# Optimization experiments

Measured on AMD Instinct MI355X. Metric: run time of the kernel, lower is better.

The kernel has to match this reference:

```python
import jax, jax.numpy as jnp
import numpy as np

NUM_JOINTS = 33
EPS = 1e-5
# MediaPipe 33-landmark pose skeleton connections
SKELETON_EDGES = np.array([
    [0,1],[1,2],[2,3],[3,7],[0,4],[4,5],[5,6],[6,8],[9,10],
    [11,12],[11,13],[13,15],[15,17],[15,19],[15,21],[17,19],
    [12,14],[14,16],[16,18],[16,20],[16,22],[18,20],
    [11,23],[12,24],[23,24],[23,25],[24,26],[25,27],[26,28],
    [27,29],[28,30],[29,31],[30,32],[27,31],[28,32]], dtype=np.int64)


def _batched_edges(B):
    und = np.concatenate([SKELETON_EDGES, SKELETON_EDGES[:, ::-1]], axis=0)
    loops = np.stack([np.arange(NUM_JOINTS)] * 2, axis=1)
    e = np.concatenate([und, loops], axis=0)  # [103, 2] per graph (incl. self loops)
    eb = (e[None, :, :] + (np.arange(B) * NUM_JOINTS)[:, None, None]).reshape(-1, 2)
    return jnp.asarray(eb[:, 0], dtype=jnp.int32), jnp.asarray(eb[:, 1], dtype=jnp.int32)


def setup_inputs() -> dict:
    key = jax.random.key(0)
    B, N, F, H, L = 4096, NUM_JOINTS, 256, 256, 4
    ks = jax.random.split(key, 20)
    d = {"x": jax.random.normal(ks[0], (B, N, F), dtype=jnp.float32)}
    dims = [(F, H), (H, H), (H, H)]
    i = 1
    for li, (di, do) in enumerate(dims):
        d[f"w{li}"] = jax.random.normal(ks[i], (di, do), dtype=jnp.float32) * 0.05; i += 1
        d[f"b{li}"] = jnp.zeros((do,), dtype=jnp.float32)
        d[f"g{li}"] = jnp.ones((do,), dtype=jnp.float32)
        d[f"be{li}"] = jnp.zeros((do,), dtype=jnp.float32)
    d["wh"] = jax.random.normal(ks[i], (H, H), dtype=jnp.float32) * 0.05; i += 1
    d["bh"] = jnp.zeros((H,), dtype=jnp.float32)
    d["wc"] = jax.random.normal(ks[i], (H, L), dtype=jnp.float32) * 0.05; i += 1
    d["bc"] = jnp.zeros((L,), dtype=jnp.float32)
    src, dst = _batched_edges(B)
    d["src"], d["dst"] = src, dst
    return d


def _gcn_conv(x, W, b, src, dst, norm, num_nodes):
    h = x @ W                          # [NN, out]
    msg = h[src] * norm[:, None]       # gather + scale
    agg = jax.ops.segment_sum(msg, dst, num_segments=num_nodes)
    return agg + b


def _bn_relu(x, g, be):
    mu = jnp.mean(x, axis=0)
    var = jnp.mean((x - mu) ** 2, axis=0)  # biased, torch training BN
    return jax.nn.relu((x - mu) * jax.lax.rsqrt(var + EPS) * g + be)


def reference(x, w0, b0, g0, be0, w1, b1, g1, be1, w2, b2, g2, be2, wh, bh, wc, bc, src, dst):
    B, N, F = x.shape
    NN = B * N
    h = jnp.nan_to_num(x.reshape(NN, F))
    # symmetric GCN normalization D^{-1/2}(A+I)D^{-1/2}; self loops already in edge list
    deg = jax.ops.segment_sum(jnp.ones_like(src, dtype=h.dtype), dst, num_segments=NN)
    dinv = jax.lax.rsqrt(deg)
    norm = dinv[src] * dinv[dst]
    for W, b, g, be in ((w0, b0, g0, be0), (w1, b1, g1, be1), (w2, b2, g2, be2)):
        h = _gcn_conv(h, W, b, src, dst, norm, NN)
        h = _bn_relu(h, g, be)  # dropout: eval mode -> identity
    h = _gcn_conv(h, wh, bh, src, dst, norm, NN)
    pooled = h.reshape(B, N, -1).mean(axis=1)  # global mean pool per graph
    return pooled @ wc + bc
```

## Files before the change

kernel.cpp:

```cpp
#include <hip/hip_runtime.h>

typedef unsigned short u16;
typedef __attribute__((ext_vector_type(8))) short short8;
typedef __attribute__((ext_vector_type(4))) float floatx4;

#define NN_TOT 135168

#define WAITVM(N) asm volatile("s_waitcnt vmcnt(" #N ")" ::: "memory")
#define WAITLGKM0 asm volatile("s_waitcnt lgkmcnt(0)" ::: "memory")

static constexpr int NBCNT[33] = {2,2,2,2,2,2,2,1,1,1,1,3,3,2,2,4,4,2,2,2,2,1,1,3,3,2,2,3,3,2,2,2,2};
static constexpr int NBR[33][4] = {
 {1,4,0,0},{0,2,0,0},{1,3,0,0},{2,7,0,0},{0,5,0,0},{4,6,0,0},{5,8,0,0},
 {3,0,0,0},{6,0,0,0},{10,0,0,0},{9,0,0,0},
 {12,13,23,0},{11,14,24,0},{11,15,0,0},{12,16,0,0},
 {13,17,19,21},{14,18,20,22},
 {15,19,0,0},{16,20,0,0},{15,17,0,0},{16,18,0,0},{15,0,0,0},{16,0,0,0},
 {11,24,25,0},{12,23,26,0},{23,27,0,0},{24,28,0,0},
 {25,29,31,0},{26,30,32,0},{27,31,0,0},{28,32,0,0},{29,27,0,0},{30,28,0,0}};
static constexpr float R2 = 0.70710678f, R3 = 0.57735027f, R4 = 0.5f, R5 = 0.44721360f;
static constexpr float DINV[33] = {R3,R3,R3,R3,R3,R3,R3, R2,R2,R2,R2, R4,R4, R3,R3, R5,R5,
                                   R3,R3,R3,R3, R2,R2, R4,R4, R3,R3, R4,R4, R3,R3,R3,R3};

__device__ __forceinline__ float bf2f(u16 u) {
  unsigned int v = ((unsigned int)u) << 16; float f; __builtin_memcpy(&f, &v, 4); return f;
}
__device__ __forceinline__ u16 f2bf(float f) {
  unsigned int u; __builtin_memcpy(&u, &f, 4);
  return (u16)((u + 0x7fffu + ((u >> 16) & 1u)) >> 16);
}
__device__ __forceinline__ float ldin(const void* p, int i, int isbf) {
  return isbf ? bf2f(((const u16*)p)[i]) : ((const float*)p)[i];
}
__device__ __forceinline__ void gload_lds16(const u16* g, u16* l) {
  __builtin_amdgcn_global_load_lds((const __attribute__((address_space(1))) unsigned int*)g,
                                   (__attribute__((address_space(3))) unsigned int*)l, 16, 0, 0);
}
__device__ __forceinline__ int lof(int row, int qq) {
  return row*32 + ((qq ^ ((row >> 1) & 3)) * 8);
}

__global__ __launch_bounds__(256) void detect_kernel(const u16* __restrict__ x,
                                                     int* __restrict__ flag)
{
  __shared__ int cnt[256];
  const int t = threadIdx.x;
  int c = 0;
  for (int j = 0; j < 16; ++j) {
    u16 u = x[(t*16 + j)*2];
    int e = (u >> 7) & 0xFF;
    c += (e >= 118 && e <= 130) ? 1 : 0;
  }
  cnt[t] = c;
  __syncthreads();
  if (t == 0) {
    int s = 0;
    for (int i = 0; i < 256; ++i) s += cnt[i];
    *flag = (s > 2048) ? 1 : 0;
  }
}

__global__ __launch_bounds__(256) void transpose_kernel(const void* __restrict__ w0,
    const void* __restrict__ w1, const void* __restrict__ w2, u16* __restrict__ Wt,
    const int* __restrict__ flag)
{
  const int m = blockIdx.x >> 4;
  const int nb = (blockIdx.x & 15) * 16;
  const void* W = m == 0 ? w0 : (m == 1 ? w1 : w2);
  u16* O = Wt + (size_t)m * 65536;
  const int t = threadIdx.x;
  const int lane = t & 63, wv = t >> 6;
  const int isbf = *flag;
  if (isbf) {
    const u16* Wb = (const u16*)W;
#pragma unroll
    for (int nn = 0; nn < 4; ++nn) {
      const int n = nb + nn*4 + wv;
#pragma unroll
      for (int j = 0; j < 4; ++j) {
        const int k = lane + 64*j;
        O[n*256 + k] = Wb[k*256 + n];
      }
    }
  } else {
    const float* Wf = (const float*)W;
#pragma unroll
    for (int nn = 0; nn < 4; ++nn) {
      const int n = nb + nn*4 + wv;
#pragma unroll
      for (int j = 0; j < 4; ++j) {
        const int k = lane + 64*j;
        O[n*256 + k] = f2bf(Wf[k*256 + n]);
      }
    }
  }
}

__global__ __launch_bounds__(256) void init_kernel(const void* __restrict__ wh,
    const void* __restrict__ bh, const void* __restrict__ wc, const void* __restrict__ bc,
    float* __restrict__ wq, float* __restrict__ bq, float* __restrict__ repl,
    const int* __restrict__ flag)
{
  const int idx = blockIdx.x*256 + threadIdx.x;
  for (int i = idx; i < 3*64*512; i += 65*256) repl[i] = 0.f;
  const int isbf = *flag;
  const int t = threadIdx.x;
  const int lane = t & 63;
  if (blockIdx.x < 64) {
    const int r = blockIdx.x*4 + (t >> 6);
    float a0=0.f, a1=0.f, a2=0.f, a3=0.f;
#pragma unroll
    for (int j = 0; j < 4; ++j) {
      const int k = lane + 64*j;
      const float w = ldin(wh, r*256 + k, isbf);
      a0 += w*ldin(wc, k*4+0, isbf); a1 += w*ldin(wc, k*4+1, isbf);
      a2 += w*ldin(wc, k*4+2, isbf); a3 += w*ldin(wc, k*4+3, isbf);
    }
#pragma unroll
    for (int off = 32; off; off >>= 1) {
      a0 += __shfl_xor(a0, off); a1 += __shfl_xor(a1, off);
      a2 += __shfl_xor(a2, off); a3 += __shfl_xor(a3, off);
    }
    if (lane == 0) { wq[r*4+0]=a0; wq[r*4+1]=a1; wq[r*4+2]=a2; wq[r*4+3]=a3; }
  } else if (t < 64) {
    float s0=0.f, s1=0.f, s2=0.f, s3=0.f;
#pragma unroll
    for (int j = 0; j < 4; ++j) {
      const int k = lane + 64*j;
      const float b = ldin(bh, k, isbf);
      s0 += b*ldin(wc, k*4+0, isbf); s1 += b*ldin(wc, k*4+1, isbf);
      s2 += b*ldin(wc, k*4+2, isbf); s3 += b*ldin(wc, k*4+3, isbf);
    }
#pragma unroll
    for (int off = 32; off; off >>= 1) {
      s0 += __shfl_xor(s0, off); s1 += __shfl_xor(s1, off);
      s2 += __shfl_xor(s2, off); s3 += __shfl_xor(s3, off);
    }
    if (lane == 0) {
      bq[0] = s0 + ldin(bc, 0, isbf); bq[1] = s1 + ldin(bc, 1, isbf);
      bq[2] = s2 + ldin(bc, 2, isbf); bq[3] = s3 + ldin(bc, 3, isbf);
    }
  }
}

template<int ACT>
__global__ __launch_bounds__(256, 2) void fused_kernel(
    const void* __restrict__ Ag, const u16* __restrict__ Bt,
    const float* __restrict__ fscale, const float* __restrict__ fshift,
    const void* __restrict__ bias, u16* __restrict__ H,
    float* __restrict__ repl, const int* __restrict__ flag)
{
  __shared__ __align__(16) u16 smem[22528];
  u16* const sA0 = smem;
  u16* const sA1 = smem + 3072;
  u16* const sB0 = smem + 6144;
  u16* const sB1 = smem + 14336;
  const int tid = threadIdx.x;
  const int lane = tid & 63, w = tid >> 6;
  const int gi = w >> 1, h = w & 1;
  const int fr = lane & 15, q = lane >> 4;
  const int lr = lane >> 2, cq = lane & 3;
  const int swz = (lr >> 1) & 3;
  const int r0 = tid >> 2;
  const int c8 = (tid & 3) * 8;
  const size_t R0 = (size_t)blockIdx.x * 66;
  const int dtf = *flag;
  const int isbf = (ACT == 0) ? dtf : 1;

  const u16* Ab = (const u16*)Ag;
  const float* Af = (const float*)Ag;

  floatx4 acc[3][8];
#pragma unroll
  for (int t = 0; t < 3; ++t)
#pragma unroll
    for (int j = 0; j < 8; ++j) acc[t][j] = (floatx4){0.f, 0.f, 0.f, 0.f};

  auto issueB = [&](u16* dst, int k0) {
#pragma unroll
    for (int i = 0; i < 4; ++i)
      gload_lds16(Bt + (w*64 + i*16 + lr)*256 + k0 + (cq ^ swz)*8,
                  dst + (w*64 + i*16)*32);
  };
  auto issueA_dma = [&](u16* dst, int k0) {
    gload_lds16(Ab + (R0 + w*16 + lr)*256 + k0 + (cq ^ swz)*8, dst + (w*16)*32);
    if (w == 0) {
      size_t rg = R0 + 64 + lr;
      if (rg >= NN_TOT) rg = NN_TOT - 1;
      gload_lds16(Ab + rg*256 + k0 + (cq ^ swz)*8, dst + 64*32);
    }
  };

  uint4 regA, regA2;
  float sc8[8], sh8[8];
  auto issueA_reg = [&](int k0) {
    float4 t0 = *(const float4*)(fscale + k0 + c8);
    float4 t1 = *(const float4*)(fscale + k0 + c8 + 4);
    float4 t2 = *(const float4*)(fshift + k0 + c8);
    float4 t3 = *(const float4*)(fshift + k0 + c8 + 4);
    sc8[0]=t0.x; sc8[1]=t0.y; sc8[2]=t0.z; sc8[3]=t0.w;
    sc8[4]=t1.x; sc8[5]=t1.y; sc8[6]=t1.z; sc8[7]=t1.w;
    sh8[0]=t2.x; sh8[1]=t2.y; sh8[2]=t2.z; sh8[3]=t2.w;
    sh8[4]=t3.x; sh8[5]=t3.y; sh8[6]=t3.z; sh8[7]=t3.w;
    regA = *(const uint4*)(Ab + (R0 + r0)*256 + k0 + c8);
    if (tid >= 248)
      regA2 = *(const uint4*)(Ab + (R0 + 64 + ((tid - 248) >> 2))*256 + k0 + c8);
  };
  auto writeA = [&](u16* dst) {
    {
      const u16* us = (const u16*)&regA;
      u16 ov[8];
#pragma unroll
      for (int j = 0; j < 8; ++j) {
        float f = bf2f(us[j]);
        f = fmaxf(0.f, fmaf(f, sc8[j], sh8[j]));
        ov[j] = f2bf(f);
      }
      *(uint4*)(dst + r0*32 + ((cq ^ ((r0 >> 1) & 3))*8)) = *(const uint4*)ov;
    }
    if (tid >= 248) {
      const int rr = 64 + ((tid - 248) >> 2);
      const u16* us = (const u16*)&regA2;
      u16 ov[8];
#pragma unroll
      for (int j = 0; j < 8; ++j) {
        float f = bf2f(us[j]);
        f = fmaxf(0.f, fmaf(f, sc8[j], sh8[j]));
        ov[j] = f2bf(f);
      }
      *(uint4*)(dst + rr*32 + ((cq ^ ((rr >> 1) & 3))*8)) = *(const uint4*)ov;
    }
  };

  auto compute = [&](const u16* cA, const u16* cB) {
    short8 a[3], b[8];
#pragma unroll
    for (int t = 0; t < 3; ++t)
      a[t] = *(const short8*)(cA + lof(gi*33 + t*16 + fr, q));
#pragma unroll
    for (int nf = 0; nf < 8; ++nf)
      b[nf] = *(const short8*)(cB + lof(h*128 + nf*16 + fr, q));
#pragma unroll
    for (int t = 0; t < 3; ++t)
#pragma unroll
      for (int nf = 0; nf < 8; ++nf)
        acc[t][nf] = __builtin_amdgcn_mfma_f32_16x16x32_bf16(a[t], b[nf], acc[t][nf], 0, 0, 0);
  };

  if (ACT == 0 && !isbf) {
    for (int kc = 0; kc < 8; ++kc) {
      const int k0 = kc * 32;
      __syncthreads();
      {
        const float* ap = Af + (R0 + r0)*256 + k0 + c8;
        float4 p0 = *(const float4*)(ap);
        float4 p1 = *(const float4*)(ap + 4);
        u16 ov[8];
        ov[0]=f2bf(p0.x); ov[1]=f2bf(p0.y); ov[2]=f2bf(p0.z); ov[3]=f2bf(p0.w);
        ov[4]=f2bf(p1.x); ov[5]=f2bf(p1.y); ov[6]=f2bf(p1.z); ov[7]=f2bf(p1.w);
        *(uint4*)(sA0 + r0*32 + ((cq ^ ((r0 >> 1) & 3))*8)) = *(const uint4*)ov;
      }
      if (tid < 8) {
        const int rr = 64 + (tid >> 2);
        const float* ap = Af + (R0 + rr)*256 + k0 + c8;
        float4 p0 = *(const float4*)(ap);
        float4 p1 = *(const float4*)(ap + 4);
        u16 ov[8];
        ov[0]=f2bf(p0.x); ov[1]=f2bf(p0.y); ov[2]=f2bf(p0.z); ov[3]=f2bf(p0.w);
        ov[4]=f2bf(p1.x); ov[5]=f2bf(p1.y); ov[6]=f2bf(p1.z); ov[7]=f2bf(p1.w);
        *(uint4*)(sA0 + rr*32 + ((cq ^ ((rr >> 1) & 3))*8)) = *(const uint4*)ov;
      }
      issueB(sB0, k0);
      __syncthreads();
      compute(sA0, sB0);
    }
  } else {
    if (ACT == 0) issueA_dma(sA0, 0); else issueA_reg(0);
    issueB(sB0, 0);
    if (ACT == 1) { WAITVM(4); writeA(sA0); WAITLGKM0; }

    for (int kc = 0; kc < 8; ++kc) {
      u16* curA = (kc & 1) ? sA1 : sA0;
      u16* nxtA = (kc & 1) ? sA0 : sA1;
      u16* curB = (kc & 1) ? sB1 : sB0;
      u16* nxtB = (kc & 1) ? sB0 : sB1;
      if (kc < 7) {
        if (ACT == 0) issueA_dma(nxtA, (kc + 1) * 32);
        else          issueA_reg((kc + 1) * 32);
        issueB(nxtB, (kc + 1) * 32);
      }
      if (kc < 7) {
        if (ACT == 0) { if (w == 0) { WAITVM(6); } else { WAITVM(5); } }
        else          { if (w == 3) { WAITVM(10); } else { WAITVM(9); } }
      } else { WAITVM(0); }
      __builtin_amdgcn_sched_barrier(0);
      __builtin_amdgcn_s_barrier();

      compute(curA, curB);

      if (ACT == 1 && kc < 7) { WAITVM(4); writeA(nxtA); }
      WAITLGKM0;
    }
  }

  __syncthreads();
  u16* const Tl = smem;
#pragma unroll
  for (int t = 0; t < 3; ++t)
#pragma unroll
    for (int nf = 0; nf < 8; ++nf)
#pragma unroll
      for (int r = 0; r < 4; ++r) {
        const int row = t*16 + q*4 + r;
        if (row < 33)
          Tl[(gi*33 + row)*264 + h*128 + nf*16 + fr] = f2bf(acc[t][nf][r]);
      }
  __syncthreads();

  const int g2 = tid >> 7, cp = tid & 127;
  const size_t Gg = (size_t)blockIdx.x*2 + g2;
  float a0[33], a1[33];
#pragma unroll
  for (int d = 0; d < 33; ++d) { a0[d] = 0.f; a1[d] = 0.f; }
#pragma unroll
  for (int s = 0; s < 33; ++s) {
    const unsigned int pk = *(const unsigned int*)(Tl + (g2*33 + s)*264 + cp*2);
    const float v0 = bf2f((u16)(pk & 0xffffu)) * DINV[s];
    const float v1 = bf2f((u16)(pk >> 16)) * DINV[s];
    a0[s] += v0; a1[s] += v1;
#pragma unroll
    for (int i = 0; i < NBCNT[s]; ++i) { a0[NBR[s][i]] += v0; a1[NBR[s][i]] += v1; }
  }
  const float bv0 = ldin(bias, cp*2,     dtf);
  const float bv1 = ldin(bias, cp*2 + 1, dtf);
  float s10 = 0.f, s20 = 0.f, s11 = 0.f, s21 = 0.f;
  u16* hg = H + Gg * (33*256);
#pragma unroll
  for (int d = 0; d < 33; ++d) {
    const float o0 = fmaf(a0[d], DINV[d], bv0);
    const float o1 = fmaf(a1[d], DINV[d], bv1);
    const unsigned int pw = (unsigned int)f2bf(o0) | ((unsigned int)f2bf(o1) << 16);
    *(unsigned int*)(hg + d*256 + cp*2) = pw;
    s10 += o0; s20 += o0*o0; s11 += o1; s21 += o1*o1;
  }
  float* r1p = repl + (Gg & 63)*512;
  atomicAdd(r1p + cp*2,           s10);
  atomicAdd(r1p + cp*2 + 1,       s11);
  atomicAdd(r1p + 256 + cp*2,     s20);
  atomicAdd(r1p + 256 + cp*2 + 1, s21);
}

__global__ __launch_bounds__(256) void statfin_kernel(const float* __restrict__ repl,
    const void* __restrict__ gamma, const void* __restrict__ beta, float* __restrict__ fs,
    const int* __restrict__ flag)
{
  const int c = threadIdx.x;
  const int isbf = *flag;
  float s1 = 0.f, s2 = 0.f;
  for (int r = 0; r < 64; ++r) { s1 += repl[r*512 + c]; s2 += repl[r*512 + 256 + c]; }
  const float inv = 1.f / (float)NN_TOT;
  const float mu = s1 * inv;
  const float var = s2 * inv - mu*mu;
  const float rs = rsqrtf(var + 1e-5f);
  const float sc = rs * ldin(gamma, c, isbf);
  fs[c] = sc;
  fs[256 + c] = ldin(beta, c, isbf) - mu * sc;
}

__global__ __launch_bounds__(256) void final_kernel(const u16* __restrict__ H,
    const float* __restrict__ fs, const float* __restrict__ wq,
    const float* __restrict__ bq, void* __restrict__ outp,
    const int* __restrict__ flag)
{
  const int g = blockIdx.x, c = threadIdx.x;
  const int isbf = *flag;
  const float sc = fs[c], sh = fs[256 + c];
  const u16* hg = H + (size_t)g * (33*256);
  float v = 0.f;
#pragma unroll
  for (int s = 0; s < 33; ++s) {
    float a = DINV[s];
#pragma unroll
    for (int i = 0; i < NBCNT[s]; ++i) a += DINV[NBR[s][i]];
    const float w = DINV[s] * a * (1.f/33.f);
    float x = bf2f(hg[s*256 + c]);
    x = fmaxf(0.f, fmaf(x, sc, sh));
    v += w * x;
  }
  float p0 = v*wq[c*4+0], p1 = v*wq[c*4+1], p2 = v*wq[c*4+2], p3 = v*wq[c*4+3];
#pragma unroll
  for (int off = 32; off; off >>= 1) {
    p0 += __shfl_xor(p0, off);
    p1 += __shfl_xor(p1, off);
    p2 += __shfl_xor(p2, off);
    p3 += __shfl_xor(p3, off);
  }
  __shared__ float sred[4][4];
  const int lane = c & 63, wid = c >> 6;
  if (lane == 0) { sred[wid][0]=p0; sred[wid][1]=p1; sred[wid][2]=p2; sred[wid][3]=p3; }
  __syncthreads();
  if (c < 4) {
    float r = sred[0][c] + sred[1][c] + sred[2][c] + sred[3][c] + bq[c];
    if (isbf) ((u16*)outp)[(size_t)g*4 + c] = f2bf(r);
    else      ((float*)outp)[(size_t)g*4 + c] = r;
  }
}

extern "C" void kernel_launch(void* const* d_in, const int* in_sizes, int n_in,
                              void* d_out, int out_size, void* d_ws, size_t ws_size,
                              hipStream_t stream)
{
  const void* x   = d_in[0];
  const void* w0  = d_in[1];
  const void* b0  = d_in[2];
  const void* g0  = d_in[3];
  const void* be0 = d_in[4];
  const void* w1  = d_in[5];
  const void* b1  = d_in[6];
  const void* g1  = d_in[7];
  const void* be1 = d_in[8];
  const void* w2  = d_in[9];
  const void* b2  = d_in[10];
  const void* g2  = d_in[11];
  const void* be2 = d_in[12];
  const void* wh  = d_in[13];
  const void* bh  = d_in[14];
  const void* wc  = d_in[15];
  const void* bc  = d_in[16];

  char* ws = (char*)d_ws;
  float* wq   = (float*)(ws + 0);
  float* bq   = (float*)(ws + 4096);
  float* fs   = (float*)(ws + 4608);
  int*   flag = (int*)  (ws + 12288);
  float* repl = (float*)(ws + 16384);
  u16*   Wt   = (u16*)  (ws + 409600);
  u16*   A    = (u16*)  (ws + 802816);
  (void)in_sizes; (void)n_in; (void)out_size; (void)ws_size;

  detect_kernel<<<1, 256, 0, stream>>>((const u16*)x, flag);
  transpose_kernel<<<48, 256, 0, stream>>>(w0, w1, w2, Wt, flag);
  init_kernel<<<65, 256, 0, stream>>>(wh, bh, wc, bc, wq, bq, repl, flag);

  fused_kernel<0><<<2048, 256, 0, stream>>>(x, Wt, nullptr, nullptr, b0, A, repl, flag);
  statfin_kernel<<<1, 256, 0, stream>>>(repl, g0, be0, fs, flag);
  fused_kernel<1><<<2048, 256, 0, stream>>>(A, Wt + 65536, fs, fs + 256, b1, A, repl + 32768, flag);
  statfin_kernel<<<1, 256, 0, stream>>>(repl + 32768, g1, be1, fs + 512, flag);
  fused_kernel<1><<<2048, 256, 0, stream>>>(A, Wt + 131072, fs + 512, fs + 768, b2, A, repl + 65536, flag);
  statfin_kernel<<<1, 256, 0, stream>>>(repl + 65536, g2, be2, fs + 1024, flag);
  final_kernel<<<4096, 256, 0, stream>>>(A, fs + 1024, wq, bq, d_out, flag);
}
```

Before: 423.0 us.

## Deepen A prefetch pipeline, raise occupancy, cache BN params in LDS, vectorize final

The fused GEMM kernel now uses a triple-buffered LDS A tile for the DMA path and double-buffered register prefetch for the activation path, issuing loads two k-steps ahead with retuned vmcnt waits. BN scale/shift are staged once into LDS instead of reloaded per k-step, and launch bounds ask for three blocks per CU. The final pooling kernel processes four graphs per block with one wave each, using vectorized bf16 loads and no LDS reduction. The risks are register pressure from the occupancy target, LDS growth, and fragile hand-counted wait counts.

```diff
diff --git a/kernel.cpp b/kernel.cpp
--- a/kernel.cpp
+++ b/kernel.cpp
@@ -8,6 +8,7 @@
 
 #define WAITVM(N) asm volatile("s_waitcnt vmcnt(" #N ")" ::: "memory")
 #define WAITLGKM0 asm volatile("s_waitcnt lgkmcnt(0)" ::: "memory")
+#define VMFENCE   asm volatile("" ::: "memory")
 
 static constexpr int NBCNT[33] = {2,2,2,2,2,2,2,1,1,1,1,3,3,2,2,4,4,2,2,2,2,1,1,3,3,2,2,3,3,2,2,2,2};
 static constexpr int NBR[33][4] = {
@@ -144,17 +145,13 @@
 }
 
 template<int ACT>
-__global__ __launch_bounds__(256, 2) void fused_kernel(
+__global__ __launch_bounds__(256, 3) void fused_kernel(
     const void* __restrict__ Ag, const u16* __restrict__ Bt,
     const float* __restrict__ fscale, const float* __restrict__ fshift,
     const void* __restrict__ bias, u16* __restrict__ H,
     float* __restrict__ repl, const int* __restrict__ flag)
 {
-  __shared__ __align__(16) u16 smem[22528];
-  u16* const sA0 = smem;
-  u16* const sA1 = smem + 3072;
-  u16* const sB0 = smem + 6144;
-  u16* const sB1 = smem + 14336;
+  __shared__ __align__(16) u16 smem[25184];
   const int tid = threadIdx.x;
   const int lane = tid & 63, w = tid >> 6;
   const int gi = w >> 1, h = w & 1;
@@ -166,9 +163,9 @@
   const size_t R0 = (size_t)blockIdx.x * 66;
   const int dtf = *flag;
   const int isbf = (ACT == 0) ? dtf : 1;
-
   const u16* Ab = (const u16*)Ag;
   const float* Af = (const float*)Ag;
+  float* const sS = (float*)(smem + 24160);
 
   floatx4 acc[3][8];
 #pragma unroll
@@ -176,13 +173,20 @@
 #pragma unroll
     for (int j = 0; j < 8; ++j) acc[t][j] = (floatx4){0.f, 0.f, 0.f, 0.f};
 
-  auto issueB = [&](u16* dst, int k0) {
+  auto sAbuf = [&](int i) -> u16* { return smem + i*2592; };
+  auto sBbuf = [&](int i) -> u16* { return smem + 7776 + i*8192; };
+
+  auto issueB = [&](int t) {
+    u16* dst = sBbuf(t & 1);
+    const int k0 = t * 32;
 #pragma unroll
     for (int i = 0; i < 4; ++i)
       gload_lds16(Bt + (w*64 + i*16 + lr)*256 + k0 + (cq ^ swz)*8,
                   dst + (w*64 + i*16)*32);
   };
-  auto issueA_dma = [&](u16* dst, int k0) {
+  auto issueA_dma = [&](int t) {
+    u16* dst = sAbuf(t % 3);
+    const int k0 = t * 32;
     gload_lds16(Ab + (R0 + w*16 + lr)*256 + k0 + (cq ^ swz)*8, dst + (w*16)*32);
     if (w == 0) {
       size_t rg = R0 + 64 + lr;
@@ -191,48 +195,42 @@
     }
   };
 
-  uint4 regA, regA2;
-  float sc8[8], sh8[8];
-  auto issueA_reg = [&](int k0) {
-    float4 t0 = *(const float4*)(fscale + k0 + c8);
-    float4 t1 = *(const float4*)(fscale + k0 + c8 + 4);
-    float4 t2 = *(const float4*)(fshift + k0 + c8);
-    float4 t3 = *(const float4*)(fshift + k0 + c8 + 4);
-    sc8[0]=t0.x; sc8[1]=t0.y; sc8[2]=t0.z; sc8[3]=t0.w;
-    sc8[4]=t1.x; sc8[5]=t1.y; sc8[6]=t1.z; sc8[7]=t1.w;
-    sh8[0]=t2.x; sh8[1]=t2.y; sh8[2]=t2.z; sh8[3]=t2.w;
-    sh8[4]=t3.x; sh8[5]=t3.y; sh8[6]=t3.z; sh8[7]=t3.w;
-    regA = *(const uint4*)(Ab + (R0 + r0)*256 + k0 + c8);
+  uint4 regA[2], regA2[2];
+  auto issueA_reg = [&](int t) {
+    const int k0 = t * 32;
+    regA[t & 1] = *(const uint4*)(Ab + (R0 + r0)*256 + k0 + c8);
     if (tid >= 248)
-      regA2 = *(const uint4*)(Ab + (R0 + 64 + ((tid - 248) >> 2))*256 + k0 + c8);
+      regA2[t & 1] = *(const uint4*)(Ab + (R0 + 64 + ((tid - 248) >> 2))*256 + k0 + c8);
   };
-  auto writeA = [&](u16* dst) {
+  auto writeA = [&](int t) {
+    u16* dst = sAbuf(t & 1);
+    const int k0 = t * 32;
+    const float4 s0 = *(const float4*)(sS + k0 + c8);
+    const float4 s1 = *(const float4*)(sS + k0 + c8 + 4);
+    const float4 t0 = *(const float4*)(sS + 256 + k0 + c8);
+    const float4 t1 = *(const float4*)(sS + 256 + k0 + c8 + 4);
+    const float sc[8] = {s0.x,s0.y,s0.z,s0.w, s1.x,s1.y,s1.z,s1.w};
+    const float sh[8] = {t0.x,t0.y,t0.z,t0.w, t1.x,t1.y,t1.z,t1.w};
     {
-      const u16* us = (const u16*)&regA;
+      const u16* us = (const u16*)&regA[t & 1];
       u16 ov[8];
 #pragma unroll
-      for (int j = 0; j < 8; ++j) {
-        float f = bf2f(us[j]);
-        f = fmaxf(0.f, fmaf(f, sc8[j], sh8[j]));
-        ov[j] = f2bf(f);
-      }
+      for (int j = 0; j < 8; ++j)
+        ov[j] = f2bf(fmaxf(0.f, fmaf(bf2f(us[j]), sc[j], sh[j])));
       *(uint4*)(dst + r0*32 + ((cq ^ ((r0 >> 1) & 3))*8)) = *(const uint4*)ov;
     }
     if (tid >= 248) {
       const int rr = 64 + ((tid - 248) >> 2);
-      const u16* us = (const u16*)&regA2;
+      const u16* us = (const u16*)&regA2[t & 1];
       u16 ov[8];
 #pragma unroll
-      for (int j = 0; j < 8; ++j) {
-        float f = bf2f(us[j]);
-        f = fmaxf(0.f, fmaf(f, sc8[j], sh8[j]));
-        ov[j] = f2bf(f);
-      }
+      for (int j = 0; j < 8; ++j)
+        ov[j] = f2bf(fmaxf(0.f, fmaf(bf2f(us[j]), sc[j], sh[j])));
       *(uint4*)(dst + rr*32 + ((cq ^ ((rr >> 1) & 3))*8)) = *(const uint4*)ov;
     }
   };
 
-  auto compute = [&](const u16* cA, const u16* cB) {
+  auto computeP = [&](const u16* cA, const u16* cB) {
     short8 a[3], b[8];
 #pragma unroll
     for (int t = 0; t < 3; ++t)
@@ -258,7 +256,7 @@
         u16 ov[8];
         ov[0]=f2bf(p0.x); ov[1]=f2bf(p0.y); ov[2]=f2bf(p0.z); ov[3]=f2bf(p0.w);
         ov[4]=f2bf(p1.x); ov[5]=f2bf(p1.y); ov[6]=f2bf(p1.z); ov[7]=f2bf(p1.w);
-        *(uint4*)(sA0 + r0*32 + ((cq ^ ((r0 >> 1) & 3))*8)) = *(const uint4*)ov;
+        *(uint4*)(sAbuf(0) + r0*32 + ((cq ^ ((r0 >> 1) & 3))*8)) = *(const uint4*)ov;
       }
       if (tid < 8) {
         const int rr = 64 + (tid >> 2);
@@ -268,38 +266,47 @@
         u16 ov[8];
         ov[0]=f2bf(p0.x); ov[1]=f2bf(p0.y); ov[2]=f2bf(p0.z); ov[3]=f2bf(p0.w);
         ov[4]=f2bf(p1.x); ov[5]=f2bf(p1.y); ov[6]=f2bf(p1.z); ov[7]=f2bf(p1.w);
-        *(uint4*)(sA0 + rr*32 + ((cq ^ ((rr >> 1) & 3))*8)) = *(const uint4*)ov;
-      }
-      issueB(sB0, k0);
+        *(uint4*)(sAbuf(0) + rr*32 + ((cq ^ ((rr >> 1) & 3))*8)) = *(const uint4*)ov;
+      }
+#pragma unroll
+      for (int i = 0; i < 4; ++i)
+        gload_lds16(Bt + (w*64 + i*16 + lr)*256 + k0 + (cq ^ swz)*8,
+                    sBbuf(0) + (w*64 + i*16)*32);
       __syncthreads();
-      compute(sA0, sB0);
+      computeP(sAbuf(0), sBbuf(0));
     }
   } else {
-    if (ACT == 0) issueA_dma(sA0, 0); else issueA_reg(0);
-    issueB(sB0, 0);
-    if (ACT == 1) { WAITVM(4); writeA(sA0); WAITLGKM0; }
-
+    if (ACT == 1) {
+      const float f0 = fscale[tid], f1 = fshift[tid];
+      WAITVM(0);
+      sS[tid] = f0; sS[256 + tid] = f1;
+      WAITLGKM0;
+    }
+    issueB(0);
+    VMFENCE;
+    if (ACT == 0) { issueA_dma(0); issueA_dma(1); }
+    else          { issueA_reg(0); issueA_reg(1); }
+    if (ACT == 1) {
+      __builtin_amdgcn_s_barrier();
+      writeA(0);
+      WAITLGKM0;
+    }
+    const bool sp = (ACT == 0) ? (w == 0) : (w == 3);
+#pragma unroll
     for (int kc = 0; kc < 8; ++kc) {
-      u16* curA = (kc & 1) ? sA1 : sA0;
-      u16* nxtA = (kc & 1) ? sA0 : sA1;
-      u16* curB = (kc & 1) ? sB1 : sB0;
-      u16* nxtB = (kc & 1) ? sB0 : sB1;
-      if (kc < 7) {
-        if (ACT == 0) issueA_dma(nxtA, (kc + 1) * 32);
-        else          issueA_reg((kc + 1) * 32);
-        issueB(nxtB, (kc + 1) * 32);
-      }
-      if (kc < 7) {
-        if (ACT == 0) { if (w == 0) { WAITVM(6); } else { WAITVM(5); } }
-        else          { if (w == 3) { WAITVM(10); } else { WAITVM(9); } }
-      } else { WAITVM(0); }
+      if (kc < 7) issueB(kc + 1);
+      VMFENCE;
+      if (kc < 6) { if (ACT == 0) issueA_dma(kc + 2); else issueA_reg(kc + 2); }
+      if (kc < 6)       { if (sp) { WAITVM(8); } else { WAITVM(6); } }
+      else if (kc == 6) { if (sp) { WAITVM(6); } else { WAITVM(5); } }
+      else              { WAITVM(0); }
       __builtin_amdgcn_sched_barrier(0);
       __builtin_amdgcn_s_barrier();
-
-      compute(curA, curB);
-
-      if (ACT == 1 && kc < 7) { WAITVM(4); writeA(nxtA); }
-      WAITLGKM0;
+      computeP(ACT == 0 ? sAbuf(kc % 3) : sAbuf(kc & 1), sBbuf(kc & 1));
+      if (ACT == 1 && kc < 7) {
+        writeA(kc + 1);
+        WAITLGKM0;
+      }
     }
   }
 
@@ -372,37 +379,48 @@
     const float* __restrict__ bq, void* __restrict__ outp,
     const int* __restrict__ flag)
 {
-  const int g = blockIdx.x, c = threadIdx.x;
+  const int tid = threadIdx.x;
+  const int lane = tid & 63, wv = tid >> 6;
+  const size_t g = (size_t)blockIdx.x * 4 + wv;
   const int isbf = *flag;
-  const float sc = fs[c], sh = fs[256 + c];
-  const u16* hg = H + (size_t)g * (33*256);
-  float v = 0.f;
+  const int c4 = lane * 4;
+  const float4 scv = *(const float4*)(fs + c4);
+  const float4 shv = *(const float4*)(fs + 256 + c4);
+  const u16* hg = H + g * (33*256);
+  float v0 = 0.f, v1 = 0.f, v2 = 0.f, v3 = 0.f;
 #pragma unroll
   for (int s = 0; s < 33; ++s) {
     float a = DINV[s];
 #pragma unroll
     for (int i = 0; i < NBCNT[s]; ++i) a += DINV[NBR[s][i]];
-    const float w = DINV[s] * a * (1.f/33.f);
-    float x = bf2f(hg[s*256 + c]);
-    x = fmaxf(0.f, fmaf(x, sc, sh));
-    v += w * x;
-  }
-  float p0 = v*wq[c*4+0], p1 = v*wq[c*4+1], p2 = v*wq[c*4+2], p3 = v*wq[c*4+3];
+    const float ws = DINV[s] * a * (1.f/33.f);
+    const uint2 pk = *(const uint2*)(hg + s*256 + c4);
+    v0 += ws * fmaxf(0.f, fmaf(bf2f((u16)(pk.x & 0xffffu)), scv.x, shv.x));
+    v1 += ws * fmaxf(0.f, fmaf(bf2f((u16)(pk.x >> 16)),     scv.y, shv.y));
+    v2 += ws * fmaxf(0.f, fmaf(bf2f((u16)(pk.y & 0xffffu)), scv.z, shv.z));
+    v3 += ws * fmaxf(0.f, fmaf(bf2f((u16)(pk.y >> 16)),     scv.w, shv.w));
+  }
+  const float4 q0 = *(const float4*)(wq + (c4+0)*4);
+  const float4 q1 = *(const float4*)(wq + (c4+1)*4);
+  const float4 q2 = *(const float4*)(wq + (c4+2)*4);
+  const float4 q3 = *(const float4*)(wq + (c4+3)*4);
+  float p0 = v0*q0.x + v1*q1.x + v2*q2.x + v3*q3.x;
+  float p1 = v0*q0.y + v1*q1.y + v2*q2.y + v3*q3.y;
+  float p2 = v0*q0.z + v1*q1.z + v2*q2.z + v3*q3.z;
+  float p3 = v0*q0.w + v1*q1.w + v2*q2.w + v3*q3.w;
 #pragma unroll
   for (int off = 32; off; off >>= 1) {
-    p0 += __shfl_xor(p0, off);
-    p1 += __shfl_xor(p1, off);
-    p2 += __shfl_xor(p2, off);
-    p3 += __shfl_xor(p3, off);
-  }
-  __shared__ float sred[4][4];
-  const int lane = c & 63, wid = c >> 6;
-  if (lane == 0) { sred[wid][0]=p0; sred[wid][1]=p1; sred[wid][2]=p2; sred[wid][3]=p3; }
-  __syncthreads();
-  if (c < 4) {
-    float r = sred[0][c] + sred[1][c] + sred[2][c] + sred[3][c] + bq[c];
-    if (isbf) ((u16*)outp)[(size_t)g*4 + c] = f2bf(r);
-    else      ((float*)outp)[(size_t)g*4 + c] = r;
+    p0 += __shfl_xor(p0, off); p1 += __shfl_xor(p1, off);
+    p2 += __shfl_xor(p2, off); p3 += __shfl_xor(p3, off);
+  }
+  if (lane == 0) {
+    if (isbf) {
+      u16* o = (u16*)outp + g*4;
+      o[0]=f2bf(p0+bq[0]); o[1]=f2bf(p1+bq[1]); o[2]=f2bf(p2+bq[2]); o[3]=f2bf(p3+bq[3]);
+    } else {
+      float* o = (float*)outp + g*4;
+      o[0]=p0+bq[0]; o[1]=p1+bq[1]; o[2]=p2+bq[2]; o[3]=p3+bq[3];
+    }
   }
 }
 
@@ -448,5 +466,5 @@
   statfin_kernel<<<1, 256, 0, stream>>>(repl + 32768, g1, be1, fs + 512, flag);
   fused_kernel<1><<<2048, 256, 0, stream>>>(A, Wt + 131072, fs + 512, fs + 768, b2, A, repl + 65536, flag);
   statfin_kernel<<<1, 256, 0, stream>>>(repl + 65536, g2, be2, fs + 1024, flag);
-  final_kernel<<<4096, 256, 0, stream>>>(A, fs + 1024, wq, bq, d_out, flag);
-}
+  final_kernel<<<1024, 256, 0, stream>>>(A, fs + 1024, wq, bq, d_out, flag);
+}
```

New measurement: 496.4 us. 17.4% more time.
